# Performance work log

Measured on AMD Instinct MI355X. Metric: run time of the kernel, lower is better.

## Reference

```python
import jax, jax.numpy as jnp
import numpy as np

N_HEADS = 12

def setup_inputs() -> dict:
    key = jax.random.key(0)
    k1, k2, k3 = jax.random.split(key, 3)
    B, S, W = 8, 1024, 768
    x = jax.random.normal(k1, (B, S, W), dtype=jnp.float32)
    w_qkv = jax.random.normal(k2, (W, 3 * W), dtype=jnp.float32) * (W ** -0.5)
    w_out = jax.random.normal(k3, (W, W), dtype=jnp.float32) * (W ** -0.5)
    return {"x": x, "w_qkv": w_qkv, "w_out": w_out}

def reference(x, w_qkv, w_out):
    B, S, W = x.shape
    H = N_HEADS
    D = W // H  # head_width
    scale = W ** -0.5  # NOTE: source scales by width**-0.5, not head_width**-0.5
    qkv = x @ w_qkv  # [B, S, 3W]
    q, k, v = jnp.split(qkv, 3, axis=2)
    q = q.reshape(B, S, H, D)
    k = k.reshape(B, S, H, D)
    # attn_score: [B, i, j, n]
    attn_score = jnp.einsum('binh,bjnh->bijn', q, k) * scale
    attn_weight = jax.nn.softmax(attn_score, axis=2)
    # NOTE: source uses K (not V) here — faithful reproduction of the bug.
    out = jnp.einsum('bijn,bjnh->binh', attn_weight, k)
    out = out.reshape(B, S, W)
    return out @ w_out  # dropout is identity in eval
```

## Files before the change

### kernel.cpp

```cpp
#include <hip/hip_runtime.h>

#define US unsigned short

typedef __bf16 bf16x8 __attribute__((ext_vector_type(8)));
typedef short s16x8 __attribute__((ext_vector_type(8)));
typedef short s16x4 __attribute__((ext_vector_type(4)));
typedef float f32x4 __attribute__((ext_vector_type(4)));

static __device__ __forceinline__ US f2bf(float f) {
  union { float f; unsigned u; } x; x.f = f;
  unsigned r = x.u + 0x7fffu + ((x.u >> 16) & 1u);
  return (US)(r >> 16);
}

static __device__ __forceinline__ unsigned cvtpk(float lo, float hi) {
  unsigned r;
  asm("v_cvt_pk_bf16_f32 %0, %1, %2" : "=v"(r) : "v"(lo), "v"(hi));
  return r;
}

static __device__ __forceinline__ void gload16(const US* g, US* l) {
  __builtin_amdgcn_global_load_lds(
      (const __attribute__((address_space(1))) void*)g,
      (__attribute__((address_space(3))) void*)l, 16, 0, 0);
}

__global__ __launch_bounds__(256) void prep(
    const float* __restrict__ x, const float* __restrict__ wqkv,
    const float* __restrict__ wout, US* __restrict__ xb,
    US* __restrict__ wqkT, US* __restrict__ woutT, float cexp) {
  __shared__ float t[32][33];
  const int bid = blockIdx.x, tid = threadIdx.x;
  if (bid < 3072) {
    int i = bid * 256 + tid;
    const float4* s = (const float4*)x + (size_t)i * 2;
    float4 a = s[0], b = s[1];
    s16x8 w;
    w[0] = (short)f2bf(a.x); w[1] = (short)f2bf(a.y);
    w[2] = (short)f2bf(a.z); w[3] = (short)f2bf(a.w);
    w[4] = (short)f2bf(b.x); w[5] = (short)f2bf(b.y);
    w[6] = (short)f2bf(b.z); w[7] = (short)f2bf(b.w);
    *(s16x8*)(xb + (size_t)i * 8) = w;
    return;
  }
  const float* src;
  US* dst;
  int n0, r0, C, nlim;
  float scale;
  if (bid < 4224) {
    int tb = bid - 3072;
    n0 = (tb % 48) * 32; r0 = (tb / 48) * 32;
    src = wqkv; dst = wqkT; C = 2304; nlim = 768; scale = cexp;
  } else {
    int tb = bid - 4224;
    n0 = (tb % 24) * 32; r0 = (tb / 24) * 32;
    src = wout; dst = woutT; C = 768; nlim = 0; scale = 1.0f;
  }
  const int R = 768;
  int tx = tid & 31, ty = tid >> 5;
  for (int i = 0; i < 4; ++i) {
    int r = i * 8 + ty;
    t[r][tx] = src[(size_t)(r0 + r) * C + n0 + tx];
  }
  __syncthreads();
  for (int i = 0; i < 4; ++i) {
    int n = i * 8 + ty;
    float s = (n0 + n < nlim) ? scale : 1.0f;
    dst[(size_t)(n0 + n) * R + r0 + tx] = f2bf(t[tx][n] * s);
  }
}

__global__ __launch_bounds__(256) void kt_transpose(
    const US* __restrict__ QK, US* __restrict__ KT) {
  __shared__ US t[32][34];
  int bh = blockIdx.z, b = bh / 12, h = bh % 12;
  int s0 = blockIdx.x * 32, d0 = blockIdx.y * 32;
  int tx = threadIdx.x & 31, ty = threadIdx.x >> 5;
  const US* src = QK + ((size_t)b * 1024 + s0) * 1536 + 768 + h * 64 + d0;
  for (int i = 0; i < 4; ++i)
    t[i * 8 + ty][tx] = src[(size_t)(i * 8 + ty) * 1536 + tx];
  __syncthreads();
  US* dst = KT + ((size_t)bh * 64 + d0) * 1024 + s0;
  for (int i = 0; i < 4; ++i)
    dst[(size_t)(i * 8 + ty) * 1024 + tx] = t[tx][i * 8 + ty];
}

template<int FUSE_KT>
__global__ __launch_bounds__(256) void gemm_bt(
    const US* __restrict__ A, const US* __restrict__ Bt,
    US* __restrict__ Cv, int M, int N, int K, US* __restrict__ KT) {
  __shared__ US As[2][128 * 32];
  __shared__ US Bs[2][128 * 32];
  const int tid = threadIdx.x;
  const int wave = tid >> 6, lane = tid & 63;
  const int lr = lane & 15, lg = lane >> 4;
  const int m0 = blockIdx.x * 128, n0 = blockIdx.y * 128;
  const int wr = (wave >> 1) * 64, wc = (wave & 1) * 64;
  const int srow = tid >> 2;
  const int sseg = (tid & 3) ^ (srow & 3);
  const US* gA = A + (size_t)(m0 + srow) * K + sseg * 8;
  const US* gB = Bt + (size_t)(n0 + srow) * K + sseg * 8;

  f32x4 acc[4][4];
  for (int i = 0; i < 4; ++i)
    for (int j = 0; j < 4; ++j) acc[i][j] = (f32x4){0.f, 0.f, 0.f, 0.f};

  const int nIt = K >> 5;
  for (int i = 0; i < 2; ++i) {
    gload16(gA + (size_t)i * 64 * K, &As[0][tid * 8 + i * 2048]);
    gload16(gB + (size_t)i * 64 * K, &Bs[0][tid * 8 + i * 2048]);
  }
  __syncthreads();

  for (int it = 0; it < nIt; ++it) {
    if (it + 1 < nIt) {
      int k0 = (it + 1) * 32, bb = (it + 1) & 1;
      for (int i = 0; i < 2; ++i) {
        gload16(gA + (size_t)i * 64 * K + k0, &As[bb][tid * 8 + i * 2048]);
        gload16(gB + (size_t)i * 64 * K + k0, &Bs[bb][tid * 8 + i * 2048]);
      }
    }
    const US* Ab = As[it & 1];
    const US* Bb = Bs[it & 1];
    bf16x8 af[4], bfr[4];
    for (int mi = 0; mi < 4; ++mi)
      af[mi] = *(const bf16x8*)(Ab + (wr + mi * 16 + lr) * 32 + ((lg ^ (lr & 3)) * 8));
    for (int ni = 0; ni < 4; ++ni)
      bfr[ni] = *(const bf16x8*)(Bb + (wc + ni * 16 + lr) * 32 + ((lg ^ (lr & 3)) * 8));
    for (int mi = 0; mi < 4; ++mi)
      for (int ni = 0; ni < 4; ++ni)
        acc[mi][ni] = __builtin_amdgcn_mfma_f32_16x16x32_bf16(
            af[mi], bfr[ni], acc[mi][ni], 0, 0, 0);
    __syncthreads();
  }

  for (int mi = 0; mi < 4; ++mi)
    for (int ni = 0; ni < 4; ++ni)
      for (int r = 0; r < 4; ++r) {
        size_t row = (size_t)m0 + wr + mi * 16 + lg * 4 + r;
        size_t col = (size_t)n0 + wc + ni * 16 + lr;
        Cv[row * N + col] = f2bf(acc[mi][ni][r]);
      }

  if (FUSE_KT && n0 >= 768) {
    const int h = (n0 + wc - 768) >> 6;
    const int bb = m0 >> 10;
    const int sb = (m0 & 1023) + wr + lg * 4;
    US* ktp = KT + (size_t)(bb * 12 + h) * 64 * 1024;
    for (int mi = 0; mi < 4; ++mi)
      for (int ni = 0; ni < 4; ++ni) {
        int d = ni * 16 + lr;
        s16x4 w;
        w[0] = (short)f2bf(acc[mi][ni][0]);
        w[1] = (short)f2bf(acc[mi][ni][1]);
        w[2] = (short)f2bf(acc[mi][ni][2]);
        w[3] = (short)f2bf(acc[mi][ni][3]);
        *(s16x4*)(ktp + (size_t)d * 1024 + sb + mi * 16) = w;
      }
  }
}

__global__ __launch_bounds__(256) void gemm_bt2(
    const US* __restrict__ A, const US* __restrict__ Bt,
    float* __restrict__ Cv, int M, int N, int K) {
  __shared__ US As[2][64 * 32];
  __shared__ US Bs[2][128 * 32];
  const int tid = threadIdx.x;
  const int wave = tid >> 6, lane = tid & 63;
  const int lr = lane & 15, lg = lane >> 4;
  const int m0 = blockIdx.x * 64, n0 = blockIdx.y * 128;
  const int wr = (wave >> 1) * 32, wc = (wave & 1) * 64;
  const int srow = tid >> 2;
  const int sseg = (tid & 3) ^ (srow & 3);
  const US* gA = A + (size_t)(m0 + srow) * K + sseg * 8;
  const US* gB = Bt + (size_t)(n0 + srow) * K + sseg * 8;

  f32x4 acc[2][4];
  for (int i = 0; i < 2; ++i)
    for (int j = 0; j < 4; ++j) acc[i][j] = (f32x4){0.f, 0.f, 0.f, 0.f};

  const int nIt = K >> 5;
  gload16(gA, &As[0][tid * 8]);
  for (int i = 0; i < 2; ++i)
    gload16(gB + (size_t)i * 64 * K, &Bs[0][tid * 8 + i * 2048]);
  __syncthreads();

  for (int it = 0; it < nIt; ++it) {
    if (it + 1 < nIt) {
      int k0 = (it + 1) * 32, bb = (it + 1) & 1;
      gload16(gA + k0, &As[bb][tid * 8]);
      for (int i = 0; i < 2; ++i)
        gload16(gB + (size_t)i * 64 * K + k0, &Bs[bb][tid * 8 + i * 2048]);
    }
    const US* Ab = As[it & 1];
    const US* Bb = Bs[it & 1];
    bf16x8 af[2], bfr[4];
    for (int mi = 0; mi < 2; ++mi)
      af[mi] = *(const bf16x8*)(Ab + (wr + mi * 16 + lr) * 32 + ((lg ^ (lr & 3)) * 8));
    for (int ni = 0; ni < 4; ++ni)
      bfr[ni] = *(const bf16x8*)(Bb + (wc + ni * 16 + lr) * 32 + ((lg ^ (lr & 3)) * 8));
    for (int mi = 0; mi < 2; ++mi)
      for (int ni = 0; ni < 4; ++ni)
        acc[mi][ni] = __builtin_amdgcn_mfma_f32_16x16x32_bf16(
            af[mi], bfr[ni], acc[mi][ni], 0, 0, 0);
    __syncthreads();
  }

  for (int mi = 0; mi < 2; ++mi)
    for (int ni = 0; ni < 4; ++ni)
      for (int r = 0; r < 4; ++r) {
        size_t row = (size_t)m0 + wr + mi * 16 + lg * 4 + r;
        size_t col = (size_t)n0 + wc + ni * 16 + lr;
        Cv[row * N + col] = acc[mi][ni][r];
      }
}

static __device__ __forceinline__ void softmax_route(
    const f32x4 sv[4], float& lsum, bool odd, bool hi, int laneQ0, int laneQ1,
    bf16x8& pa0v, bf16x8& pa1v) {
  float p[4][4];
#pragma unroll
  for (int ns = 0; ns < 4; ++ns)
#pragma unroll
    for (int r = 0; r < 4; ++r) {
      p[ns][r] = __builtin_amdgcn_exp2f(sv[ns][r]);
      lsum += p[ns][r];
    }
  unsigned pk00 = cvtpk(p[0][0], p[0][1]), pk01 = cvtpk(p[0][2], p[0][3]);
  unsigned pk10 = cvtpk(p[1][0], p[1][1]), pk11 = cvtpk(p[1][2], p[1][3]);
  unsigned pk20 = cvtpk(p[2][0], p[2][1]), pk21 = cvtpk(p[2][2], p[2][3]);
  unsigned pk30 = cvtpk(p[3][0], p[3][1]), pk31 = cvtpk(p[3][2], p[3][3]);
  int a0 = (int)(odd ? pk10 : pk00), a1 = (int)(odd ? pk11 : pk01);
  int a2 = (int)(odd ? pk30 : pk20), a3 = (int)(odd ? pk31 : pk21);
  int b0 = (int)(odd ? pk00 : pk10), b1 = (int)(odd ? pk01 : pk11);
  int b2 = (int)(odd ? pk20 : pk30), b3 = (int)(odd ? pk21 : pk31);
  int r0 = __shfl(a0, laneQ0), r1 = __shfl(a1, laneQ0);
  int r2 = __shfl(a2, laneQ0), r3 = __shfl(a3, laneQ0);
  int r4 = __shfl(b0, laneQ1), r5 = __shfl(b1, laneQ1);
  int r6 = __shfl(b2, laneQ1), r7 = __shfl(b3, laneQ1);
  union { unsigned u[4]; bf16x8 v; } pa0, pa1;
  pa0.u[0] = hi ? (unsigned)r4 : (unsigned)r0;
  pa0.u[1] = hi ? (unsigned)r5 : (unsigned)r1;
  pa0.u[2] = hi ? (unsigned)r0 : (unsigned)r4;
  pa0.u[3] = hi ? (unsigned)r1 : (unsigned)r5;
  pa1.u[0] = hi ? (unsigned)r6 : (unsigned)r2;
  pa1.u[1] = hi ? (unsigned)r7 : (unsigned)r3;
  pa1.u[2] = hi ? (unsigned)r2 : (unsigned)r6;
  pa1.u[3] = hi ? (unsigned)r3 : (unsigned)r7;
  pa0v = pa0.v;
  pa1v = pa1.v;
}

__global__ __launch_bounds__(256, 3) void attn_kernel(
    const US* __restrict__ QK, const US* __restrict__ KTg, US* __restrict__ AO) {
  __shared__ US Kr[2][64 * 64];
  __shared__ US Kt[2][64 * 64];
  const int tid = threadIdx.x, wave = tid >> 6, lane = tid & 63;
  const int lr = lane & 15, lg = lane >> 4;
  const int id = blockIdx.y * 8 + blockIdx.x;
  const int bh = (id & 7) * 12 + ((id >> 3) % 12);
  const int qt = id / 96;
  const int b = bh / 12, h = bh % 12;
  const int qw = qt * 128 + wave * 32;
  const size_t rowbase = (size_t)b * 1024;
  const US* Qp = QK + rowbase * 1536 + h * 64;
  const US* Kp = QK + rowbase * 1536 + 768 + h * 64;
  const US* KTp = KTg + (size_t)bh * 64 * 1024;

  const int srow = tid >> 3;
  const int sseg = (tid & 7) ^ (srow & 7);
  const US* gK = Kp + (size_t)srow * 1536 + sseg * 8;
  const US* gT = KTp + (size_t)srow * 1024 + sseg * 8;

  bf16x8 qf0[2], qf1[2];
#pragma unroll
  for (int kk = 0; kk < 2; ++kk) {
    qf0[kk] = *(const bf16x8*)(Qp + (size_t)(qw + lr) * 1536 + kk * 32 + lg * 8);
    qf1[kk] = *(const bf16x8*)(Qp + (size_t)(qw + 16 + lr) * 1536 + kk * 32 + lg * 8);
  }

  const bool odd = (lg & 1) != 0;
  const bool hi = (lg >> 1) != 0;
  const int laneQ0 = lr + 32 * (lg & 1) + 16 * (lg >> 1);
  const int laneQ1 = lr + 32 * (lg & 1) + 16 * (1 - (lg >> 1));

  float lsum0 = 0.f, lsum1 = 0.f;
  f32x4 acc0[4], acc1[4];
#pragma unroll
  for (int d = 0; d < 4; ++d) {
    acc0[d] = (f32x4){0.f, 0.f, 0.f, 0.f};
    acc1[d] = (f32x4){0.f, 0.f, 0.f, 0.f};
  }

  for (int i = 0; i < 2; ++i) {
    gload16(gK + (size_t)(i * 32) * 1536, &Kr[0][tid * 8 + i * 2048]);
    gload16(gT + (size_t)(i * 32) * 1024, &Kt[0][tid * 8 + i * 2048]);
  }
  __syncthreads();

  for (int t = 0; t < 16; ++t) {
    if (t + 1 < 16) {
      int kv0 = (t + 1) * 64, bb = (t + 1) & 1;
      for (int i = 0; i < 2; ++i) {
        gload16(gK + (size_t)(kv0 + i * 32) * 1536, &Kr[bb][tid * 8 + i * 2048]);
        gload16(gT + (size_t)(i * 32) * 1024 + kv0, &Kt[bb][tid * 8 + i * 2048]);
      }
    }
    const US* Krb = Kr[t & 1];
    const US* Ktb = Kt[t & 1];

    f32x4 sv0[4], sv1[4];
    __builtin_amdgcn_s_setprio(1);
#pragma unroll
    for (int ns = 0; ns < 4; ++ns) {
      f32x4 a0 = {0.f, 0.f, 0.f, 0.f}, a1 = {0.f, 0.f, 0.f, 0.f};
#pragma unroll
      for (int kk = 0; kk < 2; ++kk) {
        bf16x8 kf = *(const bf16x8*)(
            Krb + (ns * 16 + lr) * 64 + (((kk * 4 + lg) ^ (lr & 7)) * 8));
        a0 = __builtin_amdgcn_mfma_f32_16x16x32_bf16(kf, qf0[kk], a0, 0, 0, 0);
        a1 = __builtin_amdgcn_mfma_f32_16x16x32_bf16(kf, qf1[kk], a1, 0, 0, 0);
      }
      sv0[ns] = a0; sv1[ns] = a1;
    }
    __builtin_amdgcn_s_setprio(0);

    bf16x8 pa00, pa01, pa10, pa11;
    softmax_route(sv0, lsum0, odd, hi, laneQ0, laneQ1, pa00, pa01);
    softmax_route(sv1, lsum1, odd, hi, laneQ0, laneQ1, pa10, pa11);

    __builtin_amdgcn_s_setprio(1);
#pragma unroll
    for (int d = 0; d < 4; ++d) {
      int drow = d * 16 + lr;
      bf16x8 kf0 = *(const bf16x8*)(Ktb + drow * 64 + ((lg ^ (lr & 7)) * 8));
      bf16x8 kf1 = *(const bf16x8*)(Ktb + drow * 64 + (((4 + lg) ^ (lr & 7)) * 8));
      acc0[d] = __builtin_amdgcn_mfma_f32_16x16x32_bf16(pa00, kf0, acc0[d], 0, 0, 0);
      acc0[d] = __builtin_amdgcn_mfma_f32_16x16x32_bf16(pa01, kf1, acc0[d], 0, 0, 0);
      acc1[d] = __builtin_amdgcn_mfma_f32_16x16x32_bf16(pa10, kf0, acc1[d], 0, 0, 0);
      acc1[d] = __builtin_amdgcn_mfma_f32_16x16x32_bf16(pa11, kf1, acc1[d], 0, 0, 0);
    }
    __builtin_amdgcn_s_setprio(0);
    __syncthreads();
  }

  lsum0 += __shfl_xor(lsum0, 16);
  lsum0 += __shfl_xor(lsum0, 32);
  lsum1 += __shfl_xor(lsum1, 16);
  lsum1 += __shfl_xor(lsum1, 32);
  float inv0[4], inv1[4];
#pragma unroll
  for (int r = 0; r < 4; ++r) {
    inv0[r] = 1.0f / __shfl(lsum0, lg * 4 + r);
    inv1[r] = 1.0f / __shfl(lsum1, lg * 4 + r);
  }
#pragma unroll
  for (int d = 0; d < 4; ++d)
#pragma unroll
    for (int r = 0; r < 4; ++r) {
      size_t row0 = rowbase + qw + lg * 4 + r;
      AO[row0 * 768 + h * 64 + d * 16 + lr] = f2bf(acc0[d][r] * inv0[r]);
      size_t row1 = rowbase + qw + 16 + lg * 4 + r;
      AO[row1 * 768 + h * 64 + d * 16 + lr] = f2bf(acc1[d][r] * inv1[r]);
    }
}

extern "C" void kernel_launch(void* const* d_in, const int* in_sizes, int n_in,
                              void* d_out, int out_size, void* d_ws, size_t ws_size,
                              hipStream_t stream) {
  const float* x    = (const float*)d_in[0];
  const float* wqkv = (const float*)d_in[1];
  const float* wout = (const float*)d_in[2];
  float* out = (float*)d_out;

  US* wqkT  = (US*)d_ws;
  US* woutT = wqkT + (size_t)1536 * 768;
  US* QK    = woutT + (size_t)768 * 768;
  US* AO    = QK + (size_t)8192 * 1536;
  US* xb    = AO + (size_t)8192 * 768;
  const size_t needElems = (size_t)1536 * 768 + (size_t)768 * 768 +
                           (size_t)8192 * 1536 + (size_t)8192 * 768 * 2 +
                           (size_t)96 * 64 * 1024;
  const bool fuse = ws_size >= needElems * sizeof(US);
  US* KT = fuse ? (xb + (size_t)8192 * 768) : xb;

  const float cexp = 0.03608439182435161f * 1.4426950408889634f;

  prep<<<4800, 256, 0, stream>>>(x, wqkv, wout, xb, wqkT, woutT, cexp);
  if (fuse) {
    gemm_bt<1><<<dim3(64, 12), 256, 0, stream>>>(xb, wqkT, QK, 8192, 1536, 768, KT);
  } else {
    gemm_bt<0><<<dim3(64, 12), 256, 0, stream>>>(xb, wqkT, QK, 8192, 1536, 768, nullptr);
    kt_transpose<<<dim3(32, 2, 96), 256, 0, stream>>>(QK, KT);
  }
  attn_kernel<<<dim3(8, 96), 256, 0, stream>>>(QK, KT, AO);
  gemm_bt2<<<dim3(128, 6), 256, 0, stream>>>(AO, woutT, out, 8192, 768, 768);
}
```

Measured before the change: 99.02 us.

## Triple-buffer K tiles and software-pipeline QK of next tile with PV

Moves the K and K-transpose LDS staging from two buffers to three, so global loads run two tiles ahead. Replaces the full __syncthreads with explicit vmcnt waits plus a bare barrier. The QK MFMAs and softmax for tile t+1 are now interleaved around the PV MFMAs of tile t, to hide softmax latency and load waits. The cost is more LDS per block and extra live score registers, which could hurt occupancy.

```diff
diff --git a/kernel.cpp b/kernel.cpp
--- a/kernel.cpp
+++ b/kernel.cpp
@@ -253,8 +253,8 @@
 
 __global__ __launch_bounds__(256, 3) void attn_kernel(
     const US* __restrict__ QK, const US* __restrict__ KTg, US* __restrict__ AO) {
-  __shared__ US Kr[2][64 * 64];
-  __shared__ US Kt[2][64 * 64];
+  __shared__ US Kr[3][4096];
+  __shared__ US Kt[3][4096];
   const int tid = threadIdx.x, wave = tid >> 6, lane = tid & 63;
   const int lr = lane & 15, lg = lane >> 4;
   const int id = blockIdx.y * 8 + blockIdx.x;
@@ -292,24 +292,7 @@
     acc1[d] = (f32x4){0.f, 0.f, 0.f, 0.f};
   }
 
-  for (int i = 0; i < 2; ++i) {
-    gload16(gK + (size_t)(i * 32) * 1536, &Kr[0][tid * 8 + i * 2048]);
-    gload16(gT + (size_t)(i * 32) * 1024, &Kt[0][tid * 8 + i * 2048]);
-  }
-  __syncthreads();
-
-  for (int t = 0; t < 16; ++t) {
-    if (t + 1 < 16) {
-      int kv0 = (t + 1) * 64, bb = (t + 1) & 1;
-      for (int i = 0; i < 2; ++i) {
-        gload16(gK + (size_t)(kv0 + i * 32) * 1536, &Kr[bb][tid * 8 + i * 2048]);
-        gload16(gT + (size_t)(i * 32) * 1024 + kv0, &Kt[bb][tid * 8 + i * 2048]);
-      }
-    }
-    const US* Krb = Kr[t & 1];
-    const US* Ktb = Kt[t & 1];
-
-    f32x4 sv0[4], sv1[4];
+  auto do_qk = [&](const US* Krb, f32x4* sv0, f32x4* sv1) {
     __builtin_amdgcn_s_setprio(1);
 #pragma unroll
     for (int ns = 0; ns < 4; ++ns) {
@@ -324,11 +307,40 @@
       sv0[ns] = a0; sv1[ns] = a1;
     }
     __builtin_amdgcn_s_setprio(0);
-
-    bf16x8 pa00, pa01, pa10, pa11;
-    softmax_route(sv0, lsum0, odd, hi, laneQ0, laneQ1, pa00, pa01);
-    softmax_route(sv1, lsum1, odd, hi, laneQ0, laneQ1, pa10, pa11);
-
+  };
+
+  for (int i = 0; i < 2; ++i)
+    gload16(gK + (size_t)(i * 32) * 1536, &Kr[0][tid * 8 + i * 2048]);
+  for (int i = 0; i < 2; ++i)
+    gload16(gT + (size_t)(i * 32) * 1024, &Kt[0][tid * 8 + i * 2048]);
+  for (int i = 0; i < 2; ++i)
+    gload16(gK + (size_t)(64 + i * 32) * 1536, &Kr[1][tid * 8 + i * 2048]);
+  for (int i = 0; i < 2; ++i)
+    gload16(gT + (size_t)(i * 32) * 1024 + 64, &Kt[1][tid * 8 + i * 2048]);
+  asm volatile("s_waitcnt vmcnt(2)" ::: "memory");
+  __builtin_amdgcn_s_barrier();
+  __builtin_amdgcn_sched_barrier(0);
+
+  f32x4 sv0[4], sv1[4];
+  do_qk(Kr[0], sv0, sv1);
+  bf16x8 pa00, pa01, pa10, pa11;
+  softmax_route(sv0, lsum0, odd, hi, laneQ0, laneQ1, pa00, pa01);
+  softmax_route(sv1, lsum1, odd, hi, laneQ0, laneQ1, pa10, pa11);
+
+  int bufC = 0, bufN = 1, bufS = 2;
+  for (int t = 0; t < 16; ++t) {
+    if (t + 2 < 16) {
+      int kv0 = (t + 2) * 64;
+      for (int i = 0; i < 2; ++i)
+        gload16(gK + (size_t)(kv0 + i * 32) * 1536, &Kr[bufS][tid * 8 + i * 2048]);
+      for (int i = 0; i < 2; ++i)
+        gload16(gT + (size_t)(i * 32) * 1024 + kv0, &Kt[bufS][tid * 8 + i * 2048]);
+    }
+
+    f32x4 nsv0[4], nsv1[4];
+    if (t + 1 < 16) do_qk(Kr[bufN], nsv0, nsv1);
+
+    const US* Ktb = Kt[bufC];
     __builtin_amdgcn_s_setprio(1);
 #pragma unroll
     for (int d = 0; d < 4; ++d) {
@@ -341,7 +353,19 @@
       acc1[d] = __builtin_amdgcn_mfma_f32_16x16x32_bf16(pa11, kf1, acc1[d], 0, 0, 0);
     }
     __builtin_amdgcn_s_setprio(0);
-    __syncthreads();
+
+    if (t + 1 < 16) {
+      softmax_route(nsv0, lsum0, odd, hi, laneQ0, laneQ1, pa00, pa01);
+      softmax_route(nsv1, lsum1, odd, hi, laneQ0, laneQ1, pa10, pa11);
+    }
+
+    if (t + 2 < 16) asm volatile("s_waitcnt vmcnt(2)" ::: "memory");
+    else            asm volatile("s_waitcnt vmcnt(0)" ::: "memory");
+    __builtin_amdgcn_s_barrier();
+    __builtin_amdgcn_sched_barrier(0);
+    bufC = (bufC + 1 == 3) ? 0 : bufC + 1;
+    bufN = (bufN + 1 == 3) ? 0 : bufN + 1;
+    bufS = (bufS + 1 == 3) ? 0 : bufS + 1;
   }
 
   lsum0 += __shfl_xor(lsum0, 16);
```

After: 99.52 us. No clear change (+0.5%).
